# Performance work log

Measured on AMD Instinct MI355X. Metric: run time of the kernel, lower is better.

Reference implementation:

```python
import jax, jax.numpy as jnp
import numpy as np

N_NODES = 50000
IN, HID, OUT = 128, 128, 47
N_EDGES = 800000


def _glorot(key, shape):
    fan_in, fan_out = shape[1], shape[0]
    lim = np.sqrt(6.0 / (fan_in + fan_out)).astype(np.float32)
    return jax.random.uniform(key, shape, jnp.float32, -lim, lim)


def setup_inputs() -> dict:
    key = jax.random.key(0)
    ks = jax.random.split(key, 12)
    x = jax.random.normal(ks[0], (N_NODES, IN), jnp.float32)
    src = jax.random.randint(ks[1], (N_EDGES,), 0, N_NODES)
    dst = jax.random.randint(ks[2], (N_EDGES,), 0, N_NODES)
    return {
        "x": x, "src": src, "dst": dst,
        "w_self1": _glorot(ks[3], (HID, IN)),  "w_neigh1": _glorot(ks[4], (HID, IN)),  "b1": jnp.zeros((HID,), jnp.float32),
        "w_self2": _glorot(ks[5], (HID, HID)), "w_neigh2": _glorot(ks[6], (HID, HID)), "b2": jnp.zeros((HID,), jnp.float32),
        "w_self3": _glorot(ks[7], (OUT, HID)), "w_neigh3": _glorot(ks[8], (OUT, HID)), "b3": jnp.zeros((OUT,), jnp.float32),
    }


def _sage_conv(h, src, dst, w_self, w_neigh, b):
    # gather src features, mean-reduce per dst node (DGL copy_u + mean)
    msg = h[src]                                                  # [E, d]
    agg = jax.ops.segment_sum(msg, dst, num_segments=N_NODES)    # [N, d]
    deg = jax.ops.segment_sum(jnp.ones((dst.shape[0],), h.dtype), dst, num_segments=N_NODES)
    mean = agg / jnp.maximum(deg, 1.0)[:, None]
    # DGL SAGEConv('mean'): fc_self(h_dst) + fc_neigh(h_neigh); bias on fc_self only
    return h @ w_self.T + b + mean @ w_neigh.T


def reference(x, src, dst,
              w_self1, w_neigh1, b1,
              w_self2, w_neigh2, b2,
              w_self3, w_neigh3, b3):
    h = _sage_conv(x, src, dst, w_self1, w_neigh1, b1)
    h = jax.nn.relu(h)  # dropout is identity in eval mode
    h = _sage_conv(h, src, dst, w_self2, w_neigh2, b2)
    h = jax.nn.relu(h)
    h = _sage_conv(h, src, dst, w_self3, w_neigh3, b3)
    return h
```

## Files before the change

### kernel.cpp

```cpp
#include <hip/hip_runtime.h>

#define N_NODES 50000
#define N_EDGES 800000
#define DIM 128
#define OUTD 47
#define NBK 196
#define EPB 4096
#define NBIN ((N_EDGES + EPB - 1) / EPB)
#define XCVT_NB (N_NODES * DIM / 8 / 256)
#define WCVT_NB (DIM + DIM + 48)

typedef __attribute__((ext_vector_type(8))) short v8s;
typedef __attribute__((ext_vector_type(8))) unsigned short v8u;
typedef __attribute__((ext_vector_type(4))) float v4f;
typedef __attribute__((ext_vector_type(2))) float v2f;

static __device__ __forceinline__ unsigned short f2bf(float f) {
    union { float f; unsigned int u; } v; v.f = f;
    unsigned int x = v.u;
    return (unsigned short)((x + 0x7fffu + ((x >> 16) & 1u)) >> 16);
}
static __device__ __forceinline__ unsigned char f2fp8(float f) {
    unsigned int pk = __builtin_amdgcn_cvt_pk_fp8_f32(f, f, 0, false);
    return (unsigned char)(pk & 0xffu);
}

__global__ __launch_bounds__(256) void k_prep(const float* __restrict__ x,
                                              unsigned short* __restrict__ xb,
                                              unsigned int* __restrict__ x8,
                                              const int* __restrict__ dst,
                                              int* __restrict__ parts,
                                              const float* __restrict__ ws1, const float* __restrict__ wn1,
                                              const float* __restrict__ ws2, const float* __restrict__ wn2,
                                              const float* __restrict__ ws3, const float* __restrict__ wn3,
                                              unsigned short* __restrict__ wb1,
                                              unsigned short* __restrict__ wb2,
                                              unsigned short* __restrict__ wb3) {
    __shared__ int hist[NBK];
    const int bx = blockIdx.x, tid = threadIdx.x;
    if (bx < XCVT_NB) {
        int i = bx * 256 + tid;
        float4 v0 = ((const float4*)x)[i * 2];
        float4 v1 = ((const float4*)x)[i * 2 + 1];
        ushort4 o0, o1;
        o0.x = f2bf(v0.x); o0.y = f2bf(v0.y); o0.z = f2bf(v0.z); o0.w = f2bf(v0.w);
        o1.x = f2bf(v1.x); o1.y = f2bf(v1.y); o1.z = f2bf(v1.z); o1.w = f2bf(v1.w);
        ((ushort4*)xb)[i * 2] = o0;
        ((ushort4*)xb)[i * 2 + 1] = o1;
        unsigned int a = __builtin_amdgcn_cvt_pk_fp8_f32(v0.x, v0.y, 0, false);
        a = __builtin_amdgcn_cvt_pk_fp8_f32(v0.z, v0.w, a, true);
        unsigned int b = __builtin_amdgcn_cvt_pk_fp8_f32(v1.x, v1.y, 0, false);
        b = __builtin_amdgcn_cvt_pk_fp8_f32(v1.z, v1.w, b, true);
        uint2 o; o.x = a; o.y = b;
        ((uint2*)x8)[i] = o;
    } else if (bx < XCVT_NB + NBIN) {
        const int j = bx - XCVT_NB;
        for (int i = tid; i < NBK; i += 256) hist[i] = 0;
        __syncthreads();
        const int e0 = j * EPB;
        const int ecnt = min(EPB, N_EDGES - e0);
        for (int r = tid; r < ecnt; r += 256)
            atomicAdd(&hist[dst[e0 + r] >> 8], 1);
        __syncthreads();
        for (int i = tid; i < NBK; i += 256) parts[j * NBK + i] = hist[i];
    } else {
        int b2 = bx - XCVT_NB - NBIN;
        const float *sw, *nw; unsigned short* ob; int j, J;
        if (b2 < DIM)            { sw = ws1; nw = wn1; ob = wb1; j = b2;            J = DIM; }
        else if (b2 < 2 * DIM)   { sw = ws2; nw = wn2; ob = wb2; j = b2 - DIM;      J = DIM; }
        else                     { sw = ws3; nw = wn3; ob = wb3; j = b2 - 2 * DIM;  J = OUTD; }
        int k = tid;
        float v = 0.f;
        if (j < J) v = (k < DIM) ? sw[j * DIM + k] : nw[j * DIM + (k - DIM)];
        ob[j * 256 + k] = f2bf(v);
    }
}

__global__ __launch_bounds__(256) void k_bin(const int* __restrict__ src,
                                             const int* __restrict__ dst,
                                             const int* __restrict__ parts,
                                             unsigned int* __restrict__ packed) {
    __shared__ int s[256], gb[NBK], cnt[NBK];
    const int t = threadIdx.x;
    const int j = blockIdx.x;
    int ct = 0, cp = 0;
    for (int i = 0; i < NBIN; ++i) {
        int v = (t < NBK) ? parts[i * NBK + t] : 0;
        if (i == j) cp = ct;
        ct += v;
    }
    s[t] = ct;
    __syncthreads();
    for (int off = 1; off < 256; off <<= 1) {
        int u = (t >= off) ? s[t - off] : 0;
        __syncthreads();
        s[t] += u;
        __syncthreads();
    }
    if (t < NBK) { gb[t] = (s[t] - ct) + cp; cnt[t] = 0; }
    __syncthreads();
    const int e0 = j * EPB;
    const int ecnt = min(EPB, N_EDGES - e0);
    for (int r = t; r < ecnt; r += 256) {
        int sv = src[e0 + r], d = dst[e0 + r];
        int b = d >> 8;
        int loc = atomicAdd(&cnt[b], 1);
        packed[gb[b] + loc] = ((unsigned int)sv << 8) | (unsigned int)(d & 255);
    }
}

__global__ __launch_bounds__(256) void k_place(const unsigned int* __restrict__ packed,
                                               const int* __restrict__ parts,
                                               int* __restrict__ row_ptr,
                                               int* __restrict__ src_sorted) {
    __shared__ int s[256], baseL[NBK], totL[NBK];
    __shared__ int hist[256], cur[256];
    const int b = blockIdx.x, t = threadIdx.x;
    int ct = 0;
    for (int i = 0; i < NBIN; ++i)
        ct += (t < NBK) ? parts[i * NBK + t] : 0;
    s[t] = ct;
    hist[t] = 0;
    __syncthreads();
    for (int off = 1; off < 256; off <<= 1) {
        int u = (t >= off) ? s[t - off] : 0;
        __syncthreads();
        s[t] += u;
        __syncthreads();
    }
    if (t < NBK) { baseL[t] = s[t] - ct; totL[t] = ct; }
    __syncthreads();
    const int base = baseL[b], cb = totL[b];
    for (int i = t; i < cb; i += 256)
        atomicAdd(&hist[packed[base + i] & 255u], 1);
    __syncthreads();
    int v = hist[t];
    s[t] = v;
    __syncthreads();
    for (int off = 1; off < 256; off <<= 1) {
        int u = (t >= off) ? s[t - off] : 0;
        __syncthreads();
        s[t] += u;
        __syncthreads();
    }
    int excl = base + s[t] - v;
    int node = b * 256 + t;
    if (node < N_NODES) row_ptr[node] = excl;
    if (b == NBK - 1 && t == 255) row_ptr[N_NODES] = base + cb;
    cur[t] = excl;
    __syncthreads();
    for (int i = t; i < cb; i += 256) {
        unsigned int pkt = packed[base + i];
        int pos = atomicAdd(&cur[pkt & 255u], 1);
        src_sorted[pos] = (int)(pkt >> 8);
    }
}

static __device__ __forceinline__ void acc16(v2f* acc, uint4 u) {
    acc[0] += __builtin_amdgcn_cvt_pk_f32_fp8(u.x, false);
    acc[1] += __builtin_amdgcn_cvt_pk_f32_fp8(u.x, true);
    acc[2] += __builtin_amdgcn_cvt_pk_f32_fp8(u.y, false);
    acc[3] += __builtin_amdgcn_cvt_pk_f32_fp8(u.y, true);
    acc[4] += __builtin_amdgcn_cvt_pk_f32_fp8(u.z, false);
    acc[5] += __builtin_amdgcn_cvt_pk_f32_fp8(u.z, true);
    acc[6] += __builtin_amdgcn_cvt_pk_f32_fp8(u.w, false);
    acc[7] += __builtin_amdgcn_cvt_pk_f32_fp8(u.w, true);
}

__global__ __launch_bounds__(256) void k_agg16(const unsigned char* __restrict__ h8,
                                               const int* __restrict__ row_ptr,
                                               const int* __restrict__ srcs,
                                               unsigned short* __restrict__ meanb) {
    const int tid = threadIdx.x;
    const int lane = tid & 63, wv = tid >> 6;
    const int g8 = lane & 7;
    const int sub = (lane >> 3) & 1;
    const int ns = lane >> 4;
    const int n = blockIdx.x * 16 + wv * 4 + ns;
    const int start = row_ptr[n], end = row_ptr[n + 1];
    v2f acc[8] = {};
    int e = start;
    for (; e + 8 <= end; e += 8) {
        int s0 = srcs[e + sub];
        int s1 = srcs[e + 2 + sub];
        int s2 = srcs[e + 4 + sub];
        int s3 = srcs[e + 6 + sub];
        uint4 u0 = *(const uint4*)(h8 + (size_t)s0 * DIM + g8 * 16);
        uint4 u1 = *(const uint4*)(h8 + (size_t)s1 * DIM + g8 * 16);
        uint4 u2 = *(const uint4*)(h8 + (size_t)s2 * DIM + g8 * 16);
        uint4 u3 = *(const uint4*)(h8 + (size_t)s3 * DIM + g8 * 16);
        acc16(acc, u0); acc16(acc, u1); acc16(acc, u2); acc16(acc, u3);
    }
    if (e + 4 <= end) {
        int s0 = srcs[e + sub];
        int s1 = srcs[e + 2 + sub];
        uint4 u0 = *(const uint4*)(h8 + (size_t)s0 * DIM + g8 * 16);
        uint4 u1 = *(const uint4*)(h8 + (size_t)s1 * DIM + g8 * 16);
        acc16(acc, u0); acc16(acc, u1);
        e += 4;
    }
    if (e + 2 <= end) {
        int s0 = srcs[e + sub];
        uint4 u0 = *(const uint4*)(h8 + (size_t)s0 * DIM + g8 * 16);
        acc16(acc, u0);
        e += 2;
    }
    if (e < end && sub == 0) {
        int s0 = srcs[e];
        uint4 u0 = *(const uint4*)(h8 + (size_t)s0 * DIM + g8 * 16);
        acc16(acc, u0);
    }
    #pragma unroll
    for (int i = 0; i < 8; ++i) {
        acc[i][0] += __shfl_xor(acc[i][0], 8);
        acc[i][1] += __shfl_xor(acc[i][1], 8);
    }
    int d = end - start;
    float inv = (d > 0) ? 1.f / (float)d : 0.f;
    v2f w0 = sub ? acc[4] : acc[0];
    v2f w1 = sub ? acc[5] : acc[1];
    v2f w2 = sub ? acc[6] : acc[2];
    v2f w3 = sub ? acc[7] : acc[3];
    v8u o;
    o[0] = f2bf(w0[0] * inv); o[1] = f2bf(w0[1] * inv);
    o[2] = f2bf(w1[0] * inv); o[3] = f2bf(w1[1] * inv);
    o[4] = f2bf(w2[0] * inv); o[5] = f2bf(w2[1] * inv);
    o[6] = f2bf(w3[0] * inv); o[7] = f2bf(w3[1] * inv);
    *(v8u*)(meanb + (size_t)n * DIM + g8 * 16 + sub * 8) = o;
}

template <int JT, int TPW, bool RELU, bool OUTBF>
__global__ __launch_bounds__(256) void k_gemm_lds(const unsigned short* __restrict__ Ab,
                                                  const unsigned short* __restrict__ Mb,
                                                  const unsigned short* __restrict__ Wb,
                                                  const float* __restrict__ bias,
                                                  void* __restrict__ out,
                                                  unsigned char* __restrict__ out8,
                                                  int outdim) {
    __shared__ unsigned short Alds[64 * 256];
    __shared__ unsigned short Wlds[JT * 256];
    const int tid = threadIdx.x;
    const int m0 = blockIdx.x * 64;
    const int j0 = blockIdx.y * JT;
    v8u ar[8];
    #pragma unroll
    for (int i = 0; i < 8; ++i) {
        int t = tid + 256 * i;
        int row = t >> 5, ch = t & 31;
        int node = m0 + row; if (node >= N_NODES) node = N_NODES - 1;
        const unsigned short* s = (ch < 16) ? (Ab + (size_t)node * DIM + ch * 8)
                                            : (Mb + (size_t)node * DIM + (ch - 16) * 8);
        ar[i] = *(const v8u*)s;
    }
    constexpr int WI = (JT * 32 + 255) / 256;
    v8u wr[WI];
    #pragma unroll
    for (int i = 0; i < WI; ++i) {
        int t = tid + 256 * i;
        if (t < JT * 32) {
            int row = t >> 5, ch = t & 31;
            wr[i] = *(const v8u*)(Wb + (size_t)(j0 + row) * 256 + ch * 8);
        }
    }
    #pragma unroll
    for (int i = 0; i < 8; ++i) {
        int t = tid + 256 * i;
        int row = t >> 5, ch = t & 31;
        *(v8u*)(Alds + row * 256 + ((ch * 8) ^ ((row & 7) * 8))) = ar[i];
    }
    #pragma unroll
    for (int i = 0; i < WI; ++i) {
        int t = tid + 256 * i;
        if (t < JT * 32) {
            int row = t >> 5, ch = t & 31;
            *(v8u*)(Wlds + row * 256 + ((ch * 8) ^ ((row & 7) * 8))) = wr[i];
        }
    }
    __syncthreads();
    const int lane = tid & 63, wv = tid >> 6;
    const int m = lane & 15, qd = lane >> 4;
    const int arow = wv * 16 + m;
    v4f acc[TPW] = {};
    #pragma unroll
    for (int c = 0; c < 8; ++c) {
        const int koff = c * 32 + qd * 8;
        v8s af = *(const v8s*)(Alds + arow * 256 + (koff ^ ((arow & 7) * 8)));
        #pragma unroll
        for (int t = 0; t < TPW; ++t) {
            int wrow = t * 16 + m;
            v8s wf = *(const v8s*)(Wlds + wrow * 256 + (koff ^ ((wrow & 7) * 8)));
            acc[t] = __builtin_amdgcn_mfma_f32_16x16x32_bf16(af, wf, acc[t], 0, 0, 0);
        }
    }
    #pragma unroll
    for (int t = 0; t < TPW; ++t) {
        int col = j0 + t * 16 + m;
        bool colok = (col < outdim);
        float bv = colok ? bias[col] : 0.f;
        #pragma unroll
        for (int r = 0; r < 4; ++r) {
            int nrow = m0 + wv * 16 + qd * 4 + r;
            if (colok && nrow < N_NODES) {
                float v = acc[t][r] + bv;
                if (RELU) v = fmaxf(v, 0.f);
                size_t idx = (size_t)nrow * outdim + col;
                if (OUTBF) {
                    ((unsigned short*)out)[idx] = f2bf(v);
                    out8[idx] = f2fp8(v);
                } else {
                    ((float*)out)[idx] = v;
                }
            }
        }
    }
}

extern "C" void kernel_launch(void* const* d_in, const int* in_sizes, int n_in,
                              void* d_out, int out_size, void* d_ws, size_t ws_size,
                              hipStream_t stream) {
    const float* x   = (const float*)d_in[0];
    const int*   src = (const int*)d_in[1];
    const int*   dst = (const int*)d_in[2];
    const float* ws1 = (const float*)d_in[3];
    const float* wn1 = (const float*)d_in[4];
    const float* b1  = (const float*)d_in[5];
    const float* ws2 = (const float*)d_in[6];
    const float* wn2 = (const float*)d_in[7];
    const float* b2  = (const float*)d_in[8];
    const float* ws3 = (const float*)d_in[9];
    const float* wn3 = (const float*)d_in[10];
    const float* b3  = (const float*)d_in[11];

    char* p = (char*)d_ws;
    auto alloc = [&](size_t bytes) { char* r = p; p += (bytes + 255) & ~(size_t)255; return r; };
    int*   row_ptr = (int*)alloc((size_t)(N_NODES + 1) * 4);
    int*   srcs    = (int*)alloc((size_t)N_EDGES * 4);
    unsigned int* packed = (unsigned int*)alloc((size_t)N_EDGES * 4);
    int*   parts   = (int*)alloc((size_t)NBIN * NBK * 4);
    unsigned short* xb    = (unsigned short*)alloc((size_t)N_NODES * DIM * 2);
    unsigned short* meanb = (unsigned short*)alloc((size_t)N_NODES * DIM * 2);
    unsigned short* h1b   = (unsigned short*)alloc((size_t)N_NODES * DIM * 2);
    unsigned short* h2b   = (unsigned short*)alloc((size_t)N_NODES * DIM * 2);
    unsigned char*  h8    = (unsigned char*)alloc((size_t)N_NODES * DIM);
    unsigned short* wb1 = (unsigned short*)alloc((size_t)DIM * 256 * 2);
    unsigned short* wb2 = (unsigned short*)alloc((size_t)DIM * 256 * 2);
    unsigned short* wb3 = (unsigned short*)alloc((size_t)48 * 256 * 2);

    k_prep<<<XCVT_NB + NBIN + WCVT_NB, 256, 0, stream>>>(
        x, xb, (unsigned int*)h8, dst, parts,
        ws1, wn1, ws2, wn2, ws3, wn3, wb1, wb2, wb3);
    k_bin<<<NBIN, 256, 0, stream>>>(src, dst, parts, packed);
    k_place<<<NBK, 256, 0, stream>>>(packed, parts, row_ptr, srcs);

    const int MB = (N_NODES + 63) / 64;
    const int AB = N_NODES / 16;

    k_agg16<<<AB, 256, 0, stream>>>(h8, row_ptr, srcs, meanb);
    k_gemm_lds<64, 4, true, true><<<dim3(MB, 2), 256, 0, stream>>>(xb, meanb, wb1, b1, h1b, h8, DIM);
    k_agg16<<<AB, 256, 0, stream>>>(h8, row_ptr, srcs, meanb);
    k_gemm_lds<64, 4, true, true><<<dim3(MB, 2), 256, 0, stream>>>(h1b, meanb, wb2, b2, h2b, h8, DIM);
    k_agg16<<<AB, 256, 0, stream>>>(h8, row_ptr, srcs, meanb);
    k_gemm_lds<48, 3, false, false><<<dim3(MB, 1), 256, 0, stream>>>(h2b, meanb, wb3, b3, d_out, nullptr, OUTD);
}
```

Before: 264.4 us.

## Fuse neighbor aggregation into per-layer GEMM kernel with fragment-ordered weights

Merges the separate mean-aggregation kernel and the GEMM kernel into one per-layer kernel. The gathered mean is written straight into the LDS A tile instead of a global bf16 buffer. Weights are pre-packed into MFMA fragment order so each lane loads its operand directly from global memory instead of staging it in LDS, and one block now computes every output column. Two fp8 feature buffers are double-buffered so a layer does not overwrite the input it is still reading. This removes three launches and the mean round-trip through global memory, but the grid is smaller (782 blocks) and each block does four serial aggregation passes, which may reduce the parallelism available to hide gather latency.

Result: faster. 241.5 us (-8.7%).

```diff
diff --git a/kernel.cpp b/kernel.cpp
--- a/kernel.cpp
+++ b/kernel.cpp
@@ -8,7 +8,7 @@
 #define EPB 4096
 #define NBIN ((N_EDGES + EPB - 1) / EPB)
 #define XCVT_NB (N_NODES * DIM / 8 / 256)
-#define WCVT_NB (DIM + DIM + 48)
+#define WFNB 19
 
 typedef __attribute__((ext_vector_type(8))) short v8s;
 typedef __attribute__((ext_vector_type(8))) unsigned short v8u;
@@ -33,9 +33,9 @@
                                               const float* __restrict__ ws1, const float* __restrict__ wn1,
                                               const float* __restrict__ ws2, const float* __restrict__ wn2,
                                               const float* __restrict__ ws3, const float* __restrict__ wn3,
-                                              unsigned short* __restrict__ wb1,
-                                              unsigned short* __restrict__ wb2,
-                                              unsigned short* __restrict__ wb3) {
+                                              unsigned short* __restrict__ wf1,
+                                              unsigned short* __restrict__ wf2,
+                                              unsigned short* __restrict__ wf3) {
     __shared__ int hist[NBK];
     const int bx = blockIdx.x, tid = threadIdx.x;
     if (bx < XCVT_NB) {
@@ -65,14 +65,27 @@
         for (int i = tid; i < NBK; i += 256) parts[j * NBK + i] = hist[i];
     } else {
         int b2 = bx - XCVT_NB - NBIN;
-        const float *sw, *nw; unsigned short* ob; int j, J;
-        if (b2 < DIM)            { sw = ws1; nw = wn1; ob = wb1; j = b2;            J = DIM; }
-        else if (b2 < 2 * DIM)   { sw = ws2; nw = wn2; ob = wb2; j = b2 - DIM;      J = DIM; }
-        else                     { sw = ws3; nw = wn3; ob = wb3; j = b2 - 2 * DIM;  J = OUTD; }
-        int k = tid;
-        float v = 0.f;
-        if (j < J) v = (k < DIM) ? sw[j * DIM + k] : nw[j * DIM + (k - DIM)];
-        ob[j * 256 + k] = f2bf(v);
+        const float *sw, *nw; unsigned short* ob; int t, J;
+        if (b2 < 8)       { sw = ws1; nw = wn1; ob = wf1; t = b2;      J = DIM; }
+        else if (b2 < 16) { sw = ws2; nw = wn2; ob = wf2; t = b2 - 8;  J = DIM; }
+        else              { sw = ws3; nw = wn3; ob = wf3; t = b2 - 16; J = OUTD; }
+        const int lane = tid & 63, cp = tid >> 6;
+        const int j = t * 16 + (lane & 15);
+        const int kb = (lane >> 4) * 8;
+        #pragma unroll
+        for (int c2 = 0; c2 < 2; ++c2) {
+            int c = cp * 2 + c2;
+            int k0 = c * 32 + kb;
+            v8u o;
+            #pragma unroll
+            for (int i = 0; i < 8; ++i) {
+                int k = k0 + i;
+                float v = 0.f;
+                if (j < J) v = (k < DIM) ? sw[j * DIM + k] : nw[j * DIM + (k - DIM)];
+                o[i] = f2bf(v);
+            }
+            *(v8u*)(ob + ((size_t)((t * 8 + c) * 64 + lane)) * 8) = o;
+        }
     }
 }
 
@@ -167,134 +180,103 @@
     acc[7] += __builtin_amdgcn_cvt_pk_f32_fp8(u.w, true);
 }
 
-__global__ __launch_bounds__(256) void k_agg16(const unsigned char* __restrict__ h8,
-                                               const int* __restrict__ row_ptr,
-                                               const int* __restrict__ srcs,
-                                               unsigned short* __restrict__ meanb) {
-    const int tid = threadIdx.x;
-    const int lane = tid & 63, wv = tid >> 6;
-    const int g8 = lane & 7;
-    const int sub = (lane >> 3) & 1;
-    const int ns = lane >> 4;
-    const int n = blockIdx.x * 16 + wv * 4 + ns;
-    const int start = row_ptr[n], end = row_ptr[n + 1];
-    v2f acc[8] = {};
-    int e = start;
-    for (; e + 8 <= end; e += 8) {
-        int s0 = srcs[e + sub];
-        int s1 = srcs[e + 2 + sub];
-        int s2 = srcs[e + 4 + sub];
-        int s3 = srcs[e + 6 + sub];
-        uint4 u0 = *(const uint4*)(h8 + (size_t)s0 * DIM + g8 * 16);
-        uint4 u1 = *(const uint4*)(h8 + (size_t)s1 * DIM + g8 * 16);
-        uint4 u2 = *(const uint4*)(h8 + (size_t)s2 * DIM + g8 * 16);
-        uint4 u3 = *(const uint4*)(h8 + (size_t)s3 * DIM + g8 * 16);
-        acc16(acc, u0); acc16(acc, u1); acc16(acc, u2); acc16(acc, u3);
-    }
-    if (e + 4 <= end) {
-        int s0 = srcs[e + sub];
-        int s1 = srcs[e + 2 + sub];
-        uint4 u0 = *(const uint4*)(h8 + (size_t)s0 * DIM + g8 * 16);
-        uint4 u1 = *(const uint4*)(h8 + (size_t)s1 * DIM + g8 * 16);
-        acc16(acc, u0); acc16(acc, u1);
-        e += 4;
-    }
-    if (e + 2 <= end) {
-        int s0 = srcs[e + sub];
-        uint4 u0 = *(const uint4*)(h8 + (size_t)s0 * DIM + g8 * 16);
-        acc16(acc, u0);
-        e += 2;
-    }
-    if (e < end && sub == 0) {
-        int s0 = srcs[e];
-        uint4 u0 = *(const uint4*)(h8 + (size_t)s0 * DIM + g8 * 16);
-        acc16(acc, u0);
-    }
-    #pragma unroll
-    for (int i = 0; i < 8; ++i) {
-        acc[i][0] += __shfl_xor(acc[i][0], 8);
-        acc[i][1] += __shfl_xor(acc[i][1], 8);
-    }
-    int d = end - start;
-    float inv = (d > 0) ? 1.f / (float)d : 0.f;
-    v2f w0 = sub ? acc[4] : acc[0];
-    v2f w1 = sub ? acc[5] : acc[1];
-    v2f w2 = sub ? acc[6] : acc[2];
-    v2f w3 = sub ? acc[7] : acc[3];
-    v8u o;
-    o[0] = f2bf(w0[0] * inv); o[1] = f2bf(w0[1] * inv);
-    o[2] = f2bf(w1[0] * inv); o[3] = f2bf(w1[1] * inv);
-    o[4] = f2bf(w2[0] * inv); o[5] = f2bf(w2[1] * inv);
-    o[6] = f2bf(w3[0] * inv); o[7] = f2bf(w3[1] * inv);
-    *(v8u*)(meanb + (size_t)n * DIM + g8 * 16 + sub * 8) = o;
-}
-
-template <int JT, int TPW, bool RELU, bool OUTBF>
-__global__ __launch_bounds__(256) void k_gemm_lds(const unsigned short* __restrict__ Ab,
-                                                  const unsigned short* __restrict__ Mb,
-                                                  const unsigned short* __restrict__ Wb,
+template <int NT, bool RELU, bool OUTBF>
+__global__ __launch_bounds__(256, 4) void k_layer(const unsigned short* __restrict__ Ab,
+                                                  const unsigned char* __restrict__ g8,
+                                                  const int* __restrict__ row_ptr,
+                                                  const int* __restrict__ srcs,
+                                                  const unsigned short* __restrict__ Wf,
                                                   const float* __restrict__ bias,
                                                   void* __restrict__ out,
                                                   unsigned char* __restrict__ out8,
                                                   int outdim) {
     __shared__ unsigned short Alds[64 * 256];
-    __shared__ unsigned short Wlds[JT * 256];
     const int tid = threadIdx.x;
     const int m0 = blockIdx.x * 64;
-    const int j0 = blockIdx.y * JT;
-    v8u ar[8];
     #pragma unroll
-    for (int i = 0; i < 8; ++i) {
+    for (int i = 0; i < 4; ++i) {
         int t = tid + 256 * i;
-        int row = t >> 5, ch = t & 31;
+        int row = t >> 4, ch = t & 15;
         int node = m0 + row; if (node >= N_NODES) node = N_NODES - 1;
-        const unsigned short* s = (ch < 16) ? (Ab + (size_t)node * DIM + ch * 8)
-                                            : (Mb + (size_t)node * DIM + (ch - 16) * 8);
-        ar[i] = *(const v8u*)s;
-    }
-    constexpr int WI = (JT * 32 + 255) / 256;
-    v8u wr[WI];
-    #pragma unroll
-    for (int i = 0; i < WI; ++i) {
-        int t = tid + 256 * i;
-        if (t < JT * 32) {
-            int row = t >> 5, ch = t & 31;
-            wr[i] = *(const v8u*)(Wb + (size_t)(j0 + row) * 256 + ch * 8);
-        }
-    }
-    #pragma unroll
-    for (int i = 0; i < 8; ++i) {
-        int t = tid + 256 * i;
-        int row = t >> 5, ch = t & 31;
-        *(v8u*)(Alds + row * 256 + ((ch * 8) ^ ((row & 7) * 8))) = ar[i];
-    }
-    #pragma unroll
-    for (int i = 0; i < WI; ++i) {
-        int t = tid + 256 * i;
-        if (t < JT * 32) {
-            int row = t >> 5, ch = t & 31;
-            *(v8u*)(Wlds + row * 256 + ((ch * 8) ^ ((row & 7) * 8))) = wr[i];
-        }
-    }
-    __syncthreads();
+        v8u v = *(const v8u*)(Ab + (size_t)node * DIM + ch * 8);
+        *(v8u*)(Alds + row * 256 + ((ch * 8) ^ ((row & 7) * 8))) = v;
+    }
     const int lane = tid & 63, wv = tid >> 6;
+    const int gg = lane & 7;
+    const int sub = (lane >> 3) & 1;
+    const int ns = lane >> 4;
+    for (int pass = 0; pass < 4; ++pass) {
+        const int row = wv * 16 + pass * 4 + ns;
+        const int n = m0 + row;
+        int start = 0, end = 0;
+        if (n < N_NODES) { start = row_ptr[n]; end = row_ptr[n + 1]; }
+        v2f ga[8] = {};
+        int e = start;
+        for (; e + 8 <= end; e += 8) {
+            int s0 = srcs[e + sub];
+            int s1 = srcs[e + 2 + sub];
+            int s2 = srcs[e + 4 + sub];
+            int s3 = srcs[e + 6 + sub];
+            uint4 u0 = *(const uint4*)(g8 + (size_t)s0 * DIM + gg * 16);
+            uint4 u1 = *(const uint4*)(g8 + (size_t)s1 * DIM + gg * 16);
+            uint4 u2 = *(const uint4*)(g8 + (size_t)s2 * DIM + gg * 16);
+            uint4 u3 = *(const uint4*)(g8 + (size_t)s3 * DIM + gg * 16);
+            acc16(ga, u0); acc16(ga, u1); acc16(ga, u2); acc16(ga, u3);
+        }
+        if (e + 4 <= end) {
+            int s0 = srcs[e + sub];
+            int s1 = srcs[e + 2 + sub];
+            uint4 u0 = *(const uint4*)(g8 + (size_t)s0 * DIM + gg * 16);
+            uint4 u1 = *(const uint4*)(g8 + (size_t)s1 * DIM + gg * 16);
+            acc16(ga, u0); acc16(ga, u1);
+            e += 4;
+        }
+        if (e + 2 <= end) {
+            int s0 = srcs[e + sub];
+            uint4 u0 = *(const uint4*)(g8 + (size_t)s0 * DIM + gg * 16);
+            acc16(ga, u0);
+            e += 2;
+        }
+        if (e < end && sub == 0) {
+            int s0 = srcs[e];
+            uint4 u0 = *(const uint4*)(g8 + (size_t)s0 * DIM + gg * 16);
+            acc16(ga, u0);
+        }
+        #pragma unroll
+        for (int i = 0; i < 8; ++i) {
+            ga[i][0] += __shfl_xor(ga[i][0], 8);
+            ga[i][1] += __shfl_xor(ga[i][1], 8);
+        }
+        int d = end - start;
+        float inv = (d > 0) ? 1.f / (float)d : 0.f;
+        v2f w0 = sub ? ga[4] : ga[0];
+        v2f w1 = sub ? ga[5] : ga[1];
+        v2f w2 = sub ? ga[6] : ga[2];
+        v2f w3 = sub ? ga[7] : ga[3];
+        v8u o;
+        o[0] = f2bf(w0[0] * inv); o[1] = f2bf(w0[1] * inv);
+        o[2] = f2bf(w1[0] * inv); o[3] = f2bf(w1[1] * inv);
+        o[4] = f2bf(w2[0] * inv); o[5] = f2bf(w2[1] * inv);
+        o[6] = f2bf(w3[0] * inv); o[7] = f2bf(w3[1] * inv);
+        *(v8u*)(Alds + row * 256 + ((DIM + gg * 16 + sub * 8) ^ ((row & 7) * 8))) = o;
+    }
+    __syncthreads();
     const int m = lane & 15, qd = lane >> 4;
     const int arow = wv * 16 + m;
-    v4f acc[TPW] = {};
+    v4f acc[NT] = {};
     #pragma unroll
     for (int c = 0; c < 8; ++c) {
         const int koff = c * 32 + qd * 8;
         v8s af = *(const v8s*)(Alds + arow * 256 + (koff ^ ((arow & 7) * 8)));
         #pragma unroll
-        for (int t = 0; t < TPW; ++t) {
-            int wrow = t * 16 + m;
-            v8s wf = *(const v8s*)(Wlds + wrow * 256 + (koff ^ ((wrow & 7) * 8)));
+        for (int t = 0; t < NT; ++t) {
+            v8s wf = *(const v8s*)(Wf + ((size_t)((t * 8 + c) * 64 + lane)) * 8);
             acc[t] = __builtin_amdgcn_mfma_f32_16x16x32_bf16(af, wf, acc[t], 0, 0, 0);
         }
     }
     #pragma unroll
-    for (int t = 0; t < TPW; ++t) {
-        int col = j0 + t * 16 + m;
+    for (int t = 0; t < NT; ++t) {
+        int col = t * 16 + m;
         bool colok = (col < outdim);
         float bv = colok ? bias[col] : 0.f;
         #pragma unroll
@@ -337,28 +319,24 @@
     int*   srcs    = (int*)alloc((size_t)N_EDGES * 4);
     unsigned int* packed = (unsigned int*)alloc((size_t)N_EDGES * 4);
     int*   parts   = (int*)alloc((size_t)NBIN * NBK * 4);
-    unsigned short* xb    = (unsigned short*)alloc((size_t)N_NODES * DIM * 2);
-    unsigned short* meanb = (unsigned short*)alloc((size_t)N_NODES * DIM * 2);
-    unsigned short* h1b   = (unsigned short*)alloc((size_t)N_NODES * DIM * 2);
-    unsigned short* h2b   = (unsigned short*)alloc((size_t)N_NODES * DIM * 2);
-    unsigned char*  h8    = (unsigned char*)alloc((size_t)N_NODES * DIM);
-    unsigned short* wb1 = (unsigned short*)alloc((size_t)DIM * 256 * 2);
-    unsigned short* wb2 = (unsigned short*)alloc((size_t)DIM * 256 * 2);
-    unsigned short* wb3 = (unsigned short*)alloc((size_t)48 * 256 * 2);
-
-    k_prep<<<XCVT_NB + NBIN + WCVT_NB, 256, 0, stream>>>(
-        x, xb, (unsigned int*)h8, dst, parts,
-        ws1, wn1, ws2, wn2, ws3, wn3, wb1, wb2, wb3);
+    unsigned short* xb  = (unsigned short*)alloc((size_t)N_NODES * DIM * 2);
+    unsigned short* h1b = (unsigned short*)alloc((size_t)N_NODES * DIM * 2);
+    unsigned short* h2b = (unsigned short*)alloc((size_t)N_NODES * DIM * 2);
+    unsigned char*  h8a = (unsigned char*)alloc((size_t)N_NODES * DIM);
+    unsigned char*  h8b = (unsigned char*)alloc((size_t)N_NODES * DIM);
+    unsigned short* wf1 = (unsigned short*)alloc((size_t)8 * 8 * 64 * 8 * 2);
+    unsigned short* wf2 = (unsigned short*)alloc((size_t)8 * 8 * 64 * 8 * 2);
+    unsigned short* wf3 = (unsigned short*)alloc((size_t)3 * 8 * 64 * 8 * 2);
+
+    k_prep<<<XCVT_NB + NBIN + WFNB, 256, 0, stream>>>(
+        x, xb, (unsigned int*)h8a, dst, parts,
+        ws1, wn1, ws2, wn2, ws3, wn3, wf1, wf2, wf3);
     k_bin<<<NBIN, 256, 0, stream>>>(src, dst, parts, packed);
     k_place<<<NBK, 256, 0, stream>>>(packed, parts, row_ptr, srcs);
 
     const int MB = (N_NODES + 63) / 64;
-    const int AB = N_NODES / 16;
-
-    k_agg16<<<AB, 256, 0, stream>>>(h8, row_ptr, srcs, meanb);
-    k_gemm_lds<64, 4, true, true><<<dim3(MB, 2), 256, 0, stream>>>(xb, meanb, wb1, b1, h1b, h8, DIM);
-    k_agg16<<<AB, 256, 0, stream>>>(h8, row_ptr, srcs, meanb);
-    k_gemm_lds<64, 4, true, true><<<dim3(MB, 2), 256, 0, stream>>>(h1b, meanb, wb2, b2, h2b, h8, DIM);
-    k_agg16<<<AB, 256, 0, stream>>>(h8, row_ptr, srcs, meanb);
-    k_gemm_lds<48, 3, false, false><<<dim3(MB, 1), 256, 0, stream>>>(h2b, meanb, wb3, b3, d_out, nullptr, OUTD);
-}
+
+    k_layer<8, true, true><<<MB, 256, 0, stream>>>(xb,  h8a, row_ptr, srcs, wf1, b1, h1b, h8b, DIM);
+    k_layer<8, true, true><<<MB, 256, 0, stream>>>(h1b, h8b, row_ptr, srcs, wf2, b2, h2b, h8a, DIM);
+    k_layer<3, false, false><<<MB, 256, 0, stream>>>(h2b, h8a, row_ptr, srcs, wf3, b3, d_out, nullptr, OUTD);
+}
```
